# Optimization experiments

Measured on AMD Instinct MI355X. Metric: run time of the kernel, lower is better.

## Reference

```python
import jax, jax.numpy as jnp
import numpy as np


def setup_inputs() -> dict:
    key = jax.random.key(0)
    B, L, C = 64, 2048, 1024  # sequences, per-seq length, n_classes
    T = B * L                 # total ragged tokens
    k1, k2 = jax.random.split(key)
    outputs = jax.random.normal(k1, (T, C), dtype=jnp.float32)
    targets = jax.random.randint(k2, (T,), 0, C)
    lengths = jnp.full((B,), L, dtype=jnp.int32)  # sum(lengths) == T
    return {"outputs": outputs, "targets": targets, "lengths": lengths, "gamma": 2.0}


def reference(outputs, targets, lengths, gamma):
    T = outputs.shape[0]
    B = lengths.shape[0]
    # per-token cross-entropy, reduction='none'
    logp = jax.nn.log_softmax(outputs, axis=-1)
    loss = -jnp.take_along_axis(logp, targets[:, None], axis=1)[:, 0]  # [T]
    # ragged segment structure
    seg = jnp.repeat(jnp.arange(B), lengths, total_repeat_length=T)  # segment id per token
    starts = jnp.cumsum(lengths) - lengths                           # segment offsets
    pos = jnp.arange(T) - starts[seg]                                # position within segment
    Ls = lengths[seg]
    # linspace(-gamma, gamma, L)[pos]; L==1 -> -gamma (matches torch.linspace)
    denom = jnp.maximum(Ls - 1, 1).astype(loss.dtype)
    raw = -gamma + (2.0 * gamma) * pos.astype(loss.dtype) / denom
    # per-segment softmax; per-segment max of raw is <= gamma, subtract for stability
    e = jnp.exp(raw - gamma)
    ssum = jax.ops.segment_sum(e, seg, num_segments=B)
    w = e / ssum[seg]
    return jnp.dot(loss, w) / B
```

## Files before the change

kernel.cpp:

```cpp
#include <hip/hip_runtime.h>
#include <math.h>

#define MAXB 1024
#define NBLK 2048

__global__ void esl_setup(const int* __restrict__ lengths, int B,
                          const float* __restrict__ gamma_p,
                          int* __restrict__ starts,
                          float* __restrict__ inv_ssum) {
    const int tid = threadIdx.x;
    if (tid == 0) {
        int acc = 0;
        starts[0] = 0;
        for (int b = 0; b < B; ++b) { acc += lengths[b]; starts[b + 1] = acc; }
    }
    const float g = gamma_p[0];
    for (int b = tid; b < B; b += blockDim.x) {
        const int L = lengths[b];
        if (L <= 0) { inv_ssum[b] = 0.f; continue; }
        const int dni = (L - 1) > 1 ? (L - 1) : 1;
        const float a = 2.f * g / (float)dni;
        float ss;
        if (fabsf(a) < 1e-20f) ss = (float)L * __expf(-2.f * g);
        else ss = __expf(-2.f * g) * (expm1f(a * (float)L) / expm1f(a));
        inv_ssum[b] = 1.f / ss;
    }
}

__device__ __forceinline__ float sumexp16(const float4 v0, const float4 v1,
                                          const float4 v2, const float4 v3) {
    return __expf(v0.x) + __expf(v0.y) + __expf(v0.z) + __expf(v0.w)
         + __expf(v1.x) + __expf(v1.y) + __expf(v1.z) + __expf(v1.w)
         + __expf(v2.x) + __expf(v2.y) + __expf(v2.z) + __expf(v2.w)
         + __expf(v3.x) + __expf(v3.y) + __expf(v3.z) + __expf(v3.w);
}

__global__ __launch_bounds__(256)
void esl_main(const float* __restrict__ outputs,
              const int* __restrict__ targets,
              const int* __restrict__ lengths,
              const int* __restrict__ g_starts,
              const float* __restrict__ g_inv,
              const float* __restrict__ gamma_p,
              int T, int B, int C, int inblock,
              float* __restrict__ partials) {
    __shared__ int   sh_starts[MAXB + 1];
    __shared__ float sh_inv[MAXB];
    __shared__ float sh_part[4];

    const int tid = threadIdx.x;
    const float g = gamma_p[0];

    if (inblock) {
        if (tid < 64) {
            const int b = tid;
            const int len = (b < B) ? lengths[b] : 0;
            int sc = len;
            #pragma unroll
            for (int off = 1; off < 64; off <<= 1) {
                const int u = __shfl_up(sc, off, 64);
                if (tid >= off) sc += u;
            }
            if (b < B) {
                sh_starts[b] = sc - len;
                if (b == B - 1) sh_starts[B] = sc;
                float inv = 0.f;
                const int L = len;
                if (L > 0) {
                    const int dni = (L - 1) > 1 ? (L - 1) : 1;
                    const float a = 2.f * g / (float)dni;
                    float ss;
                    if (fabsf(a) < 1e-20f) ss = (float)L * __expf(-2.f * g);
                    else ss = __expf(-2.f * g) * (expm1f(a * (float)L) / expm1f(a));
                    inv = 1.f / ss;
                }
                sh_inv[b] = inv;
            }
        }
    } else {
        const int nb = (B < MAXB) ? B : MAXB;
        for (int i = tid; i < nb + 1; i += blockDim.x) sh_starts[i] = g_starts[i];
        for (int i = tid; i < nb;     i += blockDim.x) sh_inv[i]   = g_inv[i];
    }
    __syncthreads();

    const int wid  = tid >> 6;
    const int lane = tid & 63;
    const int* stp    = (B <= MAXB) ? sh_starts : g_starts;
    const float* invp = (B <= MAXB) ? sh_inv    : g_inv;

    float acc = 0.f;

    if (C == 1024) {
        const int nwaves = gridDim.x * 4;
        const int w = blockIdx.x * 4 + wid;
        const int npw = (T + nwaves - 1) / nwaves;
        const int tbeg = w * npw;
        const int tend = (tbeg + npw < T) ? tbeg + npw : T;

        if (tbeg < T) {
            int lo = 0, hi = B - 1;
            while (lo < hi) {
                const int mid = (lo + hi + 1) >> 1;
                if (stp[mid] <= tbeg) lo = mid; else hi = mid - 1;
            }
            int seg = lo;
            int st  = stp[seg];
            int en  = stp[seg + 1];
            float slope = 0.f, winv = 0.f;
            {
                const float dnl = fmaxf((float)(en - st) - 1.f, 1.f);
                slope = __fdividef(2.f * g, dnl);
                winv  = invp[seg];
            }
            const float n2g = -2.f * g;

            #define ESL_ADV(tt)                                                    \
                while ((tt) >= en) {                                               \
                    ++seg; st = en; en = stp[seg + 1];                             \
                    const float dnl_ = fmaxf((float)(en - st) - 1.f, 1.f);         \
                    slope = __fdividef(2.f * g, dnl_);                             \
                    winv  = invp[seg];                                             \
                }

            int t = tbeg;
            for (; t + 1 < tend; t += 2) {
                const float* rowA = outputs + (size_t)t * 1024;
                const float* rowB = rowA + 1024;
                const float4* ra = (const float4*)rowA;
                const float4* rb = (const float4*)rowB;
                const float4 a0 = ra[lane], a1 = ra[lane + 64],
                             a2 = ra[lane + 128], a3 = ra[lane + 192];
                const float4 b0 = rb[lane], b1 = rb[lane + 64],
                             b2 = rb[lane + 128], b3 = rb[lane + 192];
                const float xa = rowA[targets[t]];
                const float xb = rowB[targets[t + 1]];

                float sa = sumexp16(a0, a1, a2, a3);
                float sb = sumexp16(b0, b1, b2, b3);
                #pragma unroll
                for (int off = 32; off; off >>= 1) {
                    sa += __shfl_xor(sa, off, 64);
                    sb += __shfl_xor(sb, off, 64);
                }
                const float lseA = __logf(sa);
                const float lseB = __logf(sb);

                ESL_ADV(t);
                const float wA = __expf(fmaf((float)(t - st), slope, n2g)) * winv;
                ESL_ADV(t + 1);
                const float wB = __expf(fmaf((float)(t + 1 - st), slope, n2g)) * winv;

                acc += (lseA - xa) * wA + (lseB - xb) * wB;
            }
            if (t < tend) {
                const float* rowA = outputs + (size_t)t * 1024;
                const float4* ra = (const float4*)rowA;
                const float4 a0 = ra[lane], a1 = ra[lane + 64],
                             a2 = ra[lane + 128], a3 = ra[lane + 192];
                const float xa = rowA[targets[t]];
                float sa = sumexp16(a0, a1, a2, a3);
                #pragma unroll
                for (int off = 32; off; off >>= 1) sa += __shfl_xor(sa, off, 64);
                const float lseA = __logf(sa);
                ESL_ADV(t);
                const float wA = __expf(fmaf((float)(t - st), slope, n2g)) * winv;
                acc += (lseA - xa) * wA;
            }
            #undef ESL_ADV
        }
    } else {
        const int stride = gridDim.x * 4;
        for (int t = blockIdx.x * 4 + wid; t < T; t += stride) {
            const float* rowp = outputs + (size_t)t * (size_t)C;
            const float xt = rowp[targets[t]];
            float m = -3.402823e38f, s = 0.f;
            for (int j = lane; j < C; j += 64) m = fmaxf(m, rowp[j]);
            #pragma unroll
            for (int off = 32; off; off >>= 1) m = fmaxf(m, __shfl_xor(m, off, 64));
            for (int j = lane; j < C; j += 64) s += __expf(rowp[j] - m);
            #pragma unroll
            for (int off = 32; off; off >>= 1) s += __shfl_xor(s, off, 64);
            const float lse = m + __logf(s);
            int lo = 0, hi = B - 1;
            while (lo < hi) {
                const int mid = (lo + hi + 1) >> 1;
                if (stp[mid] <= t) lo = mid; else hi = mid - 1;
            }
            const int st  = stp[lo];
            const int L   = stp[lo + 1] - st;
            const int pos = t - st;
            const float dn  = (float)((L - 1) > 1 ? (L - 1) : 1);
            const float raw = -g + (2.f * g) * ((float)pos / dn);
            acc += (lse - xt) * __expf(raw - g) * invp[lo];
        }
    }

    if (lane == 0) sh_part[wid] = acc;
    __syncthreads();
    if (tid == 0)
        partials[blockIdx.x] = sh_part[0] + sh_part[1] + sh_part[2] + sh_part[3];
}

__global__ __launch_bounds__(256)
void esl_finish(const float* __restrict__ partials, int n, int B,
                float* __restrict__ out) {
    __shared__ float sh[4];
    float s = 0.f;
    for (int i = threadIdx.x; i < n; i += blockDim.x) s += partials[i];
    #pragma unroll
    for (int off = 32; off; off >>= 1) s += __shfl_xor(s, off, 64);
    const int wid = threadIdx.x >> 6;
    if ((threadIdx.x & 63) == 0) sh[wid] = s;
    __syncthreads();
    if (threadIdx.x == 0) out[0] = (sh[0] + sh[1] + sh[2] + sh[3]) / (float)B;
}

extern "C" void kernel_launch(void* const* d_in, const int* in_sizes, int n_in,
                              void* d_out, int out_size, void* d_ws, size_t ws_size,
                              hipStream_t stream) {
    const float* outputs = (const float*)d_in[0];
    const int*   targets = (const int*)d_in[1];
    const int*   lengths = (const int*)d_in[2];
    const float* gamma   = (const float*)d_in[3];
    float* out = (float*)d_out;

    const int T = in_sizes[1];
    const int B = in_sizes[2];
    const int C = (int)(in_sizes[0] / T);

    int*   starts   = (int*)d_ws;
    float* inv_ssum = (float*)((char*)d_ws + sizeof(int) * (size_t)(B + 1));
    float* partials = inv_ssum + B;

    const int inblock = (B <= 64) ? 1 : 0;
    if (!inblock)
        esl_setup<<<1, 256, 0, stream>>>(lengths, B, gamma, starts, inv_ssum);

    int grid = NBLK;
    const int max_needed = (T + 3) / 4;
    if (grid > max_needed) grid = max_needed;
    esl_main<<<grid, 256, 0, stream>>>(outputs, targets, lengths, starts, inv_ssum,
                                       gamma, T, B, C, inblock, partials);
    esl_finish<<<1, 256, 0, stream>>>(partials, grid, B, out);
}
```

Before: 103.4 us.

## Software-pipeline row pair loads and shuffle-broadcast targets across the wave

Restructures the C==1024 fast path into a software-pipelined loop that issues the loads for the next pair of rows before computing on the current pair. This is meant to hide global memory latency, since each wave otherwise stalls on its loads. Targets for the wave's token range are loaded once per lane and broadcast with __shfl when the range is at most 64 tokens, which drops the per-row scalar target loads. The cost is roughly double the vector registers, which may reduce occupancy, plus redundant loads on the final iteration. The segment-advance loop also gains a bounds guard.

```diff
diff --git a/kernel.cpp b/kernel.cpp
--- a/kernel.cpp
+++ b/kernel.cpp
@@ -99,6 +99,14 @@
         const int tend = (tbeg + npw < T) ? tbeg + npw : T;
 
         if (tbeg < T) {
+            const int use_shfl = (npw <= 64);
+            int tg = 0;
+            if (use_shfl) {
+                int ti = tbeg + lane;
+                if (ti > T - 1) ti = T - 1;
+                tg = targets[ti];
+            }
+
             int lo = 0, hi = B - 1;
             while (lo < hi) {
                 const int mid = (lo + hi + 1) >> 1;
@@ -107,7 +115,7 @@
             int seg = lo;
             int st  = stp[seg];
             int en  = stp[seg + 1];
-            float slope = 0.f, winv = 0.f;
+            float slope, winv;
             {
                 const float dnl = fmaxf((float)(en - st) - 1.f, 1.f);
                 slope = __fdividef(2.f * g, dnl);
@@ -116,57 +124,73 @@
             const float n2g = -2.f * g;
 
             #define ESL_ADV(tt)                                                    \
-                while ((tt) >= en) {                                               \
+                while ((tt) >= en && seg + 1 < B) {                                \
                     ++seg; st = en; en = stp[seg + 1];                             \
                     const float dnl_ = fmaxf((float)(en - st) - 1.f, 1.f);         \
                     slope = __fdividef(2.f * g, dnl_);                             \
                     winv  = invp[seg];                                             \
                 }
 
-            int t = tbeg;
-            for (; t + 1 < tend; t += 2) {
-                const float* rowA = outputs + (size_t)t * 1024;
-                const float* rowB = rowA + 1024;
-                const float4* ra = (const float4*)rowA;
-                const float4* rb = (const float4*)rowB;
-                const float4 a0 = ra[lane], a1 = ra[lane + 64],
-                             a2 = ra[lane + 128], a3 = ra[lane + 192];
-                const float4 b0 = rb[lane], b1 = rb[lane + 64],
-                             b2 = rb[lane + 128], b3 = rb[lane + 192];
-                const float xa = rowA[targets[t]];
-                const float xb = rowB[targets[t + 1]];
-
-                float sa = sumexp16(a0, a1, a2, a3);
-                float sb = sumexp16(b0, b1, b2, b3);
-                #pragma unroll
-                for (int off = 32; off; off >>= 1) {
-                    sa += __shfl_xor(sa, off, 64);
-                    sb += __shfl_xor(sb, off, 64);
-                }
-                const float lseA = __logf(sa);
-                const float lseB = __logf(sb);
-
-                ESL_ADV(t);
-                const float wA = __expf(fmaf((float)(t - st), slope, n2g)) * winv;
-                ESL_ADV(t + 1);
-                const float wB = __expf(fmaf((float)(t + 1 - st), slope, n2g)) * winv;
-
-                acc += (lseA - xa) * wA + (lseB - xb) * wB;
-            }
-            if (t < tend) {
-                const float* rowA = outputs + (size_t)t * 1024;
-                const float4* ra = (const float4*)rowA;
-                const float4 a0 = ra[lane], a1 = ra[lane + 64],
-                             a2 = ra[lane + 128], a3 = ra[lane + 192];
-                const float xa = rowA[targets[t]];
-                float sa = sumexp16(a0, a1, a2, a3);
-                #pragma unroll
-                for (int off = 32; off; off >>= 1) sa += __shfl_xor(sa, off, 64);
-                const float lseA = __logf(sa);
-                ESL_ADV(t);
-                const float wA = __expf(fmaf((float)(t - st), slope, n2g)) * winv;
-                acc += (lseA - xa) * wA;
-            }
+            #define LOADPAIR(V00,V01,V02,V03, V10,V11,V12,V13, X0, X1, tt)         \
+                do {                                                               \
+                    const int _t0 = (tt);                                          \
+                    const int _t1 = ((tt) + 1 < tend) ? (tt) + 1 : (tt);           \
+                    const float* _p0 = outputs + (size_t)_t0 * 1024;               \
+                    const float* _p1 = outputs + (size_t)_t1 * 1024;               \
+                    const float4* _q0 = (const float4*)_p0;                        \
+                    const float4* _q1 = (const float4*)_p1;                        \
+                    V00 = _q0[lane];       V01 = _q0[lane + 64];                   \
+                    V02 = _q0[lane + 128]; V03 = _q0[lane + 192];                  \
+                    V10 = _q1[lane];       V11 = _q1[lane + 64];                   \
+                    V12 = _q1[lane + 128]; V13 = _q1[lane + 192];                  \
+                    const int _c0 = use_shfl ? __shfl(tg, _t0 - tbeg, 64)          \
+                                             : targets[_t0];                       \
+                    const int _c1 = use_shfl ? __shfl(tg, _t1 - tbeg, 64)          \
+                                             : targets[_t1];                       \
+                    X0 = _p0[_c0];                                                 \
+                    X1 = _p1[_c1];                                                 \
+                } while (0)
+
+            #define COMPPAIR(V00,V01,V02,V03, V10,V11,V12,V13, X0, X1, tt)         \
+                do {                                                               \
+                    float _sa = sumexp16(V00, V01, V02, V03);                      \
+                    float _sb = sumexp16(V10, V11, V12, V13);                      \
+                    _Pragma("unroll")                                              \
+                    for (int _o = 32; _o; _o >>= 1) {                              \
+                        _sa += __shfl_xor(_sa, _o, 64);                            \
+                        _sb += __shfl_xor(_sb, _o, 64);                            \
+                    }                                                              \
+                    const float _lseA = __logf(_sa);                               \
+                    const float _lseB = __logf(_sb);                               \
+                    ESL_ADV(tt);                                                   \
+                    const float _wA =                                              \
+                        __expf(fmaf((float)((tt) - st), slope, n2g)) * winv;       \
+                    acc += (_lseA - (X0)) * _wA;                                   \
+                    if ((tt) + 1 < tend) {                                         \
+                        ESL_ADV((tt) + 1);                                         \
+                        const float _wB =                                          \
+                            __expf(fmaf((float)((tt) + 1 - st), slope, n2g))       \
+                            * winv;                                                \
+                        acc += (_lseB - (X1)) * _wB;                               \
+                    }                                                              \
+                } while (0)
+
+            float4 A0, A1, A2, A3, B0, B1, B2, B3;
+            float4 N0, N1, N2, N3, M0, M1, M2, M3;
+            float AX0, AX1, NX0, NX1;
+
+            LOADPAIR(A0, A1, A2, A3, B0, B1, B2, B3, AX0, AX1, tbeg);
+            #pragma unroll 2
+            for (int t = tbeg; t < tend; t += 2) {
+                const int tn = (t + 2 < tend) ? t + 2 : t;
+                LOADPAIR(N0, N1, N2, N3, M0, M1, M2, M3, NX0, NX1, tn);
+                COMPPAIR(A0, A1, A2, A3, B0, B1, B2, B3, AX0, AX1, t);
+                A0 = N0; A1 = N1; A2 = N2; A3 = N3;
+                B0 = M0; B1 = M1; B2 = M2; B3 = M3;
+                AX0 = NX0; AX1 = NX1;
+            }
+            #undef COMPPAIR
+            #undef LOADPAIR
             #undef ESL_ADV
         }
     } else {
```

Result: no change. 104.4 us (+1.0%).
